# Performance work log

Measured on AMD Instinct MI355X. Metric: run time of the kernel, lower is better.

Reference implementation:

```python
import jax, jax.numpy as jnp
import numpy as np

B, LP, LH, D, H = 32, 1024, 1024, 256, 256

def setup_inputs() -> dict:
    key = jax.random.key(0)
    k1, k2, k3 = jax.random.split(key, 3)
    premises = jax.random.normal(k1, (B, LP, D), dtype=jnp.float32)
    hypotheses = jax.random.normal(k2, (B, LH, D), dtype=jnp.float32)
    W_F = jax.random.normal(k3, (D, H), dtype=jnp.float32) * (1.0 / np.sqrt(D))
    return {"premises": premises, "hypotheses": hypotheses, "W_F": W_F}

def reference(premises, hypotheses, W_F):
    # Tanh-projected features: F_p = tanh(P @ W_F), F_h = tanh(H @ W_F)
    F_p = jnp.tanh(jnp.einsum('bpd,dh->bph', premises, W_F))   # [B,LP,H]
    F_h = jnp.tanh(jnp.einsum('bqd,dh->bqh', hypotheses, W_F)) # [B,LH,H]
    # Alignment scores e_ij = F_p . F_h
    eijs = jnp.einsum('bph,bqh->bpq', F_p, F_h)                # [B,LP,LH]
    # betas: for each premise token, softmax over hypothesis tokens, weighted sum of hypotheses
    betas = jnp.einsum('bpq,bqd->bpd', jax.nn.softmax(eijs, axis=-1), hypotheses)  # [B,LP,D]
    # alphas: for each hypothesis token, softmax over premise tokens, weighted sum of premises
    alphas = jnp.einsum('bqp,bpd->bqd',
                        jax.nn.softmax(jnp.swapaxes(eijs, 1, 2), axis=-1),
                        premises)                                                   # [B,LH,D]
    return betas, alphas
```

## Files before the change

kernel.cpp:

```cpp
#include <hip/hip_runtime.h>

typedef _Float16 f16;
typedef __attribute__((ext_vector_type(4))) _Float16 f16x4;
typedef __attribute__((ext_vector_type(8))) _Float16 f16x8;
typedef __attribute__((ext_vector_type(4))) float f32x4;
typedef __attribute__((ext_vector_type(16))) float f32x16;
typedef unsigned int u32;

#define BB 32
#define LL 1024
#define DD 256

__device__ __forceinline__ void async_copy16(const f16* g, f16* l) {
  __builtin_amdgcn_global_load_lds(
      (const __attribute__((address_space(1))) u32*)(const void*)g,
      (__attribute__((address_space(3))) u32*)(void*)l, 16, 0, 0);
}

__device__ __forceinline__ u32 pack_pkrtz(float a, float b) {
  auto pk = __builtin_amdgcn_cvt_pkrtz(a, b);
  u32 w;
  __builtin_memcpy(&w, &pk, 4);
  return w;
}

__global__ __launch_bounds__(256) void transpose_to_f16(
    const float* __restrict__ X0, f16* __restrict__ Y0,
    const float* __restrict__ X1, f16* __restrict__ Y1,
    int L, int D, int nbPerInput) {
  __shared__ float T[64][68];
  const int tid = threadIdx.x;
  int bz = blockIdx.z;
  const float* X = X0;
  f16* Y = Y0;
  int b = bz;
  if (bz >= nbPerInput) { X = X1; Y = Y1; b = bz - nbPerInput; }
  const int l0 = blockIdx.x * 64, d0 = blockIdx.y * 64;
  const size_t baseX = (size_t)b * L * D;
#pragma unroll
  for (int pass = 0; pass < 4; ++pass) {
    int r = (tid >> 4) + pass * 16;
    int c = (tid & 15) * 4;
    float4 v = *(const float4*)&X[baseX + (size_t)(l0 + r) * D + d0 + c];
    *(float4*)&T[r][c] = v;
  }
  __syncthreads();
  const size_t baseY = (size_t)b * D * L;
#pragma unroll
  for (int pass = 0; pass < 2; ++pass) {
    int dr = (tid >> 3) + pass * 32;
    int lc = (tid & 7) * 8;
    f16x8 o;
#pragma unroll
    for (int j = 0; j < 8; ++j) o[j] = (f16)T[lc + j][dr];
    *(f16x8*)&Y[baseY + (size_t)(d0 + dr) * L + l0 + lc] = o;
  }
}

__global__ __launch_bounds__(256, 2) void proj_mfma(
    const float* __restrict__ Pin, const float* __restrict__ Hin,
    const f16* __restrict__ Wt, f16* __restrict__ Fp, f16* __restrict__ Fh,
    f16* __restrict__ Vtp, f16* __restrict__ Vth) {
  __shared__ f16 As[64][264];
  __shared__ f16 Wts[64][264];
  const int tid = threadIdx.x;
  const int wv = tid >> 6, lane = tid & 63, quad = lane >> 4, l16 = lane & 15;
  const float* A = blockIdx.z ? Hin : Pin;
  f16* F = blockIdx.z ? Fh : Fp;
  f16* VtO = blockIdx.z ? Vth : Vtp;
  const int m0 = blockIdx.x * 64;

  {
    const int ar = tid >> 2, aq = tid & 3;
    const float* arow = A + (size_t)(m0 + ar) * 256 + aq * 64;
    f16* drow = &As[ar][aq * 64];
#pragma unroll
    for (int i = 0; i < 16; ++i) {
      float4 v = *(const float4*)&arow[i * 4];
      f16x4 bv;
      bv[0] = (f16)v.x; bv[1] = (f16)v.y; bv[2] = (f16)v.z; bv[3] = (f16)v.w;
      *(f16x4*)&drow[i * 4] = bv;
    }
  }
  __syncthreads();

  f16x8 af[8];
#pragma unroll
  for (int kc = 0; kc < 4; ++kc)
#pragma unroll
    for (int s = 0; s < 2; ++s)
      af[kc * 2 + s] =
          *(const f16x8*)&As[wv * 16 + l16][kc * 64 + s * 32 + quad * 8];

  {
    const int dd = tid & 63, lg = tid >> 6;
    const int bI = m0 >> 10, l_base = m0 & 1023;
#pragma unroll
    for (int kc = 0; kc < 4; ++kc) {
      f16* vrow =
          VtO + (size_t)bI * DD * LL + (size_t)(kc * 64 + dd) * LL + l_base;
#pragma unroll
      for (int part = 0; part < 2; ++part) {
        int lo = lg * 16 + part * 8;
        f16x8 ov;
#pragma unroll
        for (int j = 0; j < 8; ++j) ov[j] = As[lo + j][kc * 64 + dd];
        *(f16x8*)&vrow[lo] = ov;
      }
    }
  }

  for (int nc = 0; nc < 4; ++nc) {
    __syncthreads();
#pragma unroll
    for (int pass = 0; pass < 8; ++pass) {
      int row = (tid >> 5) + pass * 8;
      int chunk = tid & 31;
      *(f16x8*)&Wts[row][chunk * 8] =
          *(const f16x8*)&Wt[(size_t)(nc * 64 + row) * 256 + chunk * 8];
    }
    __syncthreads();
    f32x4 acc[4] = {};
#pragma unroll
    for (int kc = 0; kc < 4; ++kc)
#pragma unroll
      for (int s = 0; s < 2; ++s) {
#pragma unroll
        for (int t = 0; t < 4; ++t) {
          f16x8 wf =
              *(const f16x8*)&Wts[t * 16 + l16][kc * 64 + s * 32 + quad * 8];
          acc[t] = __builtin_amdgcn_mfma_f32_16x16x32_f16(af[kc * 2 + s], wf,
                                                          acc[t], 0, 0, 0);
        }
      }
#pragma unroll
    for (int t = 0; t < 4; ++t)
#pragma unroll
      for (int r = 0; r < 4; ++r) {
        float x = acc[t][r];
        float e = __expf(2.f * x);
        float th = 1.f - 2.f / (e + 1.f);
        F[(size_t)(m0 + wv * 16 + quad * 4 + r) * 256 + nc * 64 + t * 16 +
          l16] = (f16)th;
      }
  }
}

__global__ __launch_bounds__(256, 2) void flash_mfma(
    const f16* __restrict__ Fpm, const f16* __restrict__ Fhm,
    const f16* __restrict__ Vth, const f16* __restrict__ Vtp,
    float* __restrict__ Out) {
  __shared__ f16 Kf[2][16][512];
  __shared__ f16 Vf[2][16][512];

  const int tid = threadIdx.x;
  const int wv = tid >> 6, lane = tid & 63;
  const int l32 = lane & 31, half = lane >> 5;

  const f16* Fq = Fpm;
  const f16* Fk = Fhm;
  const f16* Vt = Vth;
  float* O = Out;
  if (blockIdx.y) { Fq = Fhm; Fk = Fpm; Vt = Vtp; O = Out + (size_t)BB * LL * DD; }

  const int x = blockIdx.x;
  const int b = ((x & 7) << 2) | (x >> 6);
  const int p0 = ((x >> 3) & 7) * 128 + wv * 32;
  const int p = p0 + l32;

  const f16* Fq_b = Fq + (size_t)b * LL * DD;
  const f16* Fk_b = Fk + (size_t)b * LL * DD;
  const f16* Vt_b = Vt + (size_t)b * DD * LL;

  f16x8 qf[16];
  {
    const f16* qrow = Fq_b + (size_t)p * DD + half * 8;
#pragma unroll
    for (int s = 0; s < 16; ++s) qf[s] = *(const f16x8*)&qrow[s * 16];
  }

  float m_run = -1e30f, l_run = 0.f;
  f32x16 o[8];
#pragma unroll
  for (int t = 0; t < 8; ++t) o[t] = (f32x16)(0.f);

  auto stage = [&](int buf, int q0) {
#pragma unroll
    for (int i = 0; i < 4; ++i) {
      int s = wv * 4 + i;
      async_copy16(Fk_b + (size_t)(q0 + l32) * DD + s * 16 + half * 8,
                   &Kf[buf][s][0]);
    }
#pragma unroll
    for (int i = 0; i < 4; ++i) {
      int v = wv * 4 + i;
      int t = v >> 1, h = v & 1;
      async_copy16(Vt_b + (size_t)(t * 32 + l32) * LL + q0 + h * 16 + half * 8,
                   &Vf[buf][v][0]);
    }
  };

  stage(0, 0);
  __syncthreads();

  int cur = 0;
  for (int it = 0; it < LL / 32; ++it) {
    if (it + 1 < LL / 32) stage(cur ^ 1, (it + 1) * 32);

    f32x16 S = (f32x16)(0.f);
#pragma unroll
    for (int s = 0; s < 16; ++s) {
      f16x8 kf = *(const f16x8*)&Kf[cur][s][lane * 8];
      S = __builtin_amdgcn_mfma_f32_32x32x16_f16(kf, qf[s], S, 0, 0, 0);
    }

    float mt = S[0];
#pragma unroll
    for (int r = 1; r < 16; ++r) mt = fmaxf(mt, S[r]);
    mt = fmaxf(mt, __shfl_xor(mt, 32, 64));

    const bool keep = __all((int)(mt - m_run <= 8.0f)) != 0;
    const float mn = keep ? m_run : fmaxf(m_run, mt);
    float pe[16];
    float ts = 0.f;
#pragma unroll
    for (int r = 0; r < 16; ++r) {
      pe[r] = __expf(S[r] - mn);
      ts += pe[r];
    }
    ts += __shfl_xor(ts, 32, 64);
    if (!keep) {
      const float alpha = __expf(m_run - mn);
      l_run *= alpha;
      m_run = mn;
#pragma unroll
      for (int t = 0; t < 8; ++t)
#pragma unroll
        for (int r = 0; r < 16; ++r) o[t][r] *= alpha;
    }
    l_run += ts;

    u32 pw[8];
#pragma unroll
    for (int i = 0; i < 8; ++i) pw[i] = pack_pkrtz(pe[2 * i], pe[2 * i + 1]);
    u32 rc[4];
    {
      u32 s0 = half ? pw[0] : pw[2];
      u32 s1 = half ? pw[1] : pw[3];
      u32 s2 = half ? pw[4] : pw[6];
      u32 s3 = half ? pw[5] : pw[7];
      rc[0] = (u32)__shfl_xor((int)s0, 32, 64);
      rc[1] = (u32)__shfl_xor((int)s1, 32, 64);
      rc[2] = (u32)__shfl_xor((int)s2, 32, 64);
      rc[3] = (u32)__shfl_xor((int)s3, 32, 64);
    }
    f16x8 pf[2];
#pragma unroll
    for (int h = 0; h < 2; ++h) {
      u32 tmp[4];
      tmp[0] = half ? rc[2 * h] : pw[4 * h];
      tmp[1] = half ? rc[2 * h + 1] : pw[4 * h + 1];
      tmp[2] = half ? pw[4 * h + 2] : rc[2 * h];
      tmp[3] = half ? pw[4 * h + 3] : rc[2 * h + 1];
      __builtin_memcpy(&pf[h], tmp, 16);
    }

#pragma unroll
    for (int t = 0; t < 8; ++t) {
      f16x8 v0 = *(const f16x8*)&Vf[cur][t * 2][lane * 8];
      o[t] = __builtin_amdgcn_mfma_f32_32x32x16_f16(v0, pf[0], o[t], 0, 0, 0);
      f16x8 v1 = *(const f16x8*)&Vf[cur][t * 2 + 1][lane * 8];
      o[t] = __builtin_amdgcn_mfma_f32_32x32x16_f16(v1, pf[1], o[t], 0, 0, 0);
    }

    __syncthreads();
    cur ^= 1;
  }

  const float inv = 1.f / l_run;
  float* orow = O + ((size_t)b * LL + p) * DD;
#pragma unroll
  for (int t = 0; t < 8; ++t) {
#pragma unroll
    for (int g = 0; g < 4; ++g) {
      f32x4 v;
      v[0] = o[t][4 * g + 0] * inv;
      v[1] = o[t][4 * g + 1] * inv;
      v[2] = o[t][4 * g + 2] * inv;
      v[3] = o[t][4 * g + 3] * inv;
      *(f32x4*)&orow[t * 32 + 8 * g + 4 * half] = v;
    }
  }
}

extern "C" void kernel_launch(void* const* d_in, const int* in_sizes, int n_in,
                              void* d_out, int out_size, void* d_ws,
                              size_t ws_size, hipStream_t stream) {
  const float* premises = (const float*)d_in[0];
  const float* hypotheses = (const float*)d_in[1];
  const float* W = (const float*)d_in[2];
  float* out = (float*)d_out;

  const size_t MF = (size_t)BB * LL * DD;
  f16* Fp = (f16*)d_ws;
  f16* Fh = Fp + MF;
  f16* Vth = Fh + MF;
  f16* Vtp = Vth + MF;
  f16* Wt = (f16*)((char*)d_out + (size_t)out_size * 4 - 256 * 256 * 2);

  transpose_to_f16<<<dim3(4, 4, 1), 256, 0, stream>>>(W, Wt, W, Wt, 256, 256, 1);
  proj_mfma<<<dim3(512, 1, 2), 256, 0, stream>>>(premises, hypotheses, Wt, Fp,
                                                 Fh, Vtp, Vth);
  flash_mfma<<<dim3(256, 2), 256, 0, stream>>>(Fp, Fh, Vth, Vtp, out);
}
```

Baseline: 251.1 us.

## Use 32x32 MFMA in projection, explicit vmcnt pipelining and staged output stores in flash

The projection kernel switches from 16x16x32 to 32x32x16 MFMA with a 2x2 wave tiling, changes the LDS padding and reorganizes the input load. The flash kernel replaces the per-iteration __syncthreads with explicit vmcnt waits plus raw s_barrier so the async prefetch of the next tile overlaps compute, and adds s_setprio around MFMA sections. The output epilogue goes through LDS so global stores are row-coalesced. These target LDS traffic, barrier stalls and scattered stores, at the risk of subtle sync ordering bugs (the vmcnt count must match the number of outstanding loads) and LDS bank conflicts from the 258 padding.

Measured after the change: 227.1 us. 1.11x faster.

```diff
diff --git a/kernel.cpp b/kernel.cpp
--- a/kernel.cpp
+++ b/kernel.cpp
@@ -10,6 +10,9 @@
 #define BB 32
 #define LL 1024
 #define DD 256
+
+#define VMCNT(N) asm volatile("s_waitcnt vmcnt(" #N ")" ::: "memory")
+#define LGKMCNT0 asm volatile("s_waitcnt lgkmcnt(0)" ::: "memory")
 
 __device__ __forceinline__ void async_copy16(const f16* g, f16* l) {
   __builtin_amdgcn_global_load_lds(
@@ -61,36 +64,37 @@
     const float* __restrict__ Pin, const float* __restrict__ Hin,
     const f16* __restrict__ Wt, f16* __restrict__ Fp, f16* __restrict__ Fh,
     f16* __restrict__ Vtp, f16* __restrict__ Vth) {
-  __shared__ f16 As[64][264];
-  __shared__ f16 Wts[64][264];
+  __shared__ f16 As[64][258];
+  __shared__ f16 Wts[64][258];
   const int tid = threadIdx.x;
-  const int wv = tid >> 6, lane = tid & 63, quad = lane >> 4, l16 = lane & 15;
+  const int wv = tid >> 6, lane = tid & 63;
+  const int l32 = lane & 31, half = lane >> 5;
+  const int wm = wv >> 1, wn = wv & 1;
   const float* A = blockIdx.z ? Hin : Pin;
   f16* F = blockIdx.z ? Fh : Fp;
   f16* VtO = blockIdx.z ? Vth : Vtp;
   const int m0 = blockIdx.x * 64;
 
   {
-    const int ar = tid >> 2, aq = tid & 3;
-    const float* arow = A + (size_t)(m0 + ar) * 256 + aq * 64;
-    f16* drow = &As[ar][aq * 64];
-#pragma unroll
-    for (int i = 0; i < 16; ++i) {
-      float4 v = *(const float4*)&arow[i * 4];
-      f16x4 bv;
-      bv[0] = (f16)v.x; bv[1] = (f16)v.y; bv[2] = (f16)v.z; bv[3] = (f16)v.w;
-      *(f16x4*)&drow[i * 4] = bv;
-    }
+    const int r = tid >> 4;
+    const int c4 = (tid & 15) * 4;
+#pragma unroll
+    for (int p = 0; p < 4; ++p)
+#pragma unroll
+      for (int ch = 0; ch < 4; ++ch) {
+        float4 v =
+            *(const float4*)&A[(size_t)(m0 + r + p * 16) * 256 + ch * 64 + c4];
+        f16x4 h4;
+        h4[0] = (f16)v.x; h4[1] = (f16)v.y; h4[2] = (f16)v.z; h4[3] = (f16)v.w;
+        *(f16x4*)&As[r + p * 16][ch * 64 + c4] = h4;
+      }
   }
   __syncthreads();
 
-  f16x8 af[8];
-#pragma unroll
-  for (int kc = 0; kc < 4; ++kc)
-#pragma unroll
-    for (int s = 0; s < 2; ++s)
-      af[kc * 2 + s] =
-          *(const f16x8*)&As[wv * 16 + l16][kc * 64 + s * 32 + quad * 8];
+  f16x8 af[16];
+#pragma unroll
+  for (int ks = 0; ks < 16; ++ks)
+    af[ks] = *(const f16x8*)&As[wm * 32 + l32][ks * 16 + half * 8];
 
   {
     const int dd = tid & 63, lg = tid >> 6;
@@ -120,29 +124,20 @@
           *(const f16x8*)&Wt[(size_t)(nc * 64 + row) * 256 + chunk * 8];
     }
     __syncthreads();
-    f32x4 acc[4] = {};
-#pragma unroll
-    for (int kc = 0; kc < 4; ++kc)
-#pragma unroll
-      for (int s = 0; s < 2; ++s) {
-#pragma unroll
-        for (int t = 0; t < 4; ++t) {
-          f16x8 wf =
-              *(const f16x8*)&Wts[t * 16 + l16][kc * 64 + s * 32 + quad * 8];
-          acc[t] = __builtin_amdgcn_mfma_f32_16x16x32_f16(af[kc * 2 + s], wf,
-                                                          acc[t], 0, 0, 0);
-        }
-      }
-#pragma unroll
-    for (int t = 0; t < 4; ++t)
-#pragma unroll
-      for (int r = 0; r < 4; ++r) {
-        float x = acc[t][r];
-        float e = __expf(2.f * x);
-        float th = 1.f - 2.f / (e + 1.f);
-        F[(size_t)(m0 + wv * 16 + quad * 4 + r) * 256 + nc * 64 + t * 16 +
-          l16] = (f16)th;
-      }
+    f32x16 acc = (f32x16)(0.f);
+#pragma unroll
+    for (int ks = 0; ks < 16; ++ks) {
+      f16x8 wf = *(const f16x8*)&Wts[wn * 32 + l32][ks * 16 + half * 8];
+      acc = __builtin_amdgcn_mfma_f32_32x32x16_f16(af[ks], wf, acc, 0, 0, 0);
+    }
+#pragma unroll
+    for (int r = 0; r < 16; ++r) {
+      float x = acc[r];
+      float e = __expf(2.f * x);
+      float th = 1.f - 2.f / (e + 1.f);
+      F[(size_t)(m0 + wm * 32 + (r & 3) + 8 * (r >> 2) + 4 * half) * 256 +
+        nc * 64 + wn * 32 + l32] = (f16)th;
+    }
   }
 }
 
@@ -200,19 +195,15 @@
     }
   };
 
-  stage(0, 0);
-  __syncthreads();
-
-  int cur = 0;
-  for (int it = 0; it < LL / 32; ++it) {
-    if (it + 1 < LL / 32) stage(cur ^ 1, (it + 1) * 32);
-
+  auto tile_compute = [&](int cur) {
     f32x16 S = (f32x16)(0.f);
+    __builtin_amdgcn_s_setprio(1);
 #pragma unroll
     for (int s = 0; s < 16; ++s) {
       f16x8 kf = *(const f16x8*)&Kf[cur][s][lane * 8];
       S = __builtin_amdgcn_mfma_f32_32x32x16_f16(kf, qf[s], S, 0, 0, 0);
     }
+    __builtin_amdgcn_s_setprio(0);
 
     float mt = S[0];
 #pragma unroll
@@ -265,6 +256,7 @@
       __builtin_memcpy(&pf[h], tmp, 16);
     }
 
+    __builtin_amdgcn_s_setprio(1);
 #pragma unroll
     for (int t = 0; t < 8; ++t) {
       f16x8 v0 = *(const f16x8*)&Vf[cur][t * 2][lane * 8];
@@ -272,24 +264,50 @@
       f16x8 v1 = *(const f16x8*)&Vf[cur][t * 2 + 1][lane * 8];
       o[t] = __builtin_amdgcn_mfma_f32_32x32x16_f16(v1, pf[1], o[t], 0, 0, 0);
     }
-
-    __syncthreads();
+    __builtin_amdgcn_s_setprio(0);
+  };
+
+  stage(0, 0);
+  int cur = 0;
+  for (int it = 0; it < 31; ++it) {
+    stage(cur ^ 1, (it + 1) * 32);
+    VMCNT(8);
+    __builtin_amdgcn_sched_barrier(0);
+    __builtin_amdgcn_s_barrier();
+    tile_compute(cur);
+    __builtin_amdgcn_s_barrier();
     cur ^= 1;
   }
+  VMCNT(0);
+  __builtin_amdgcn_sched_barrier(0);
+  __builtin_amdgcn_s_barrier();
+  tile_compute(cur);
+  __syncthreads();
 
   const float inv = 1.f / l_run;
-  float* orow = O + ((size_t)b * LL + p) * DD;
+  float* Tw = (float*)&Kf[0][0][0] + wv * (32 * 36);
+  float* Ob = O + (size_t)b * LL * DD;
 #pragma unroll
   for (int t = 0; t < 8; ++t) {
 #pragma unroll
     for (int g = 0; g < 4; ++g) {
+      int C = 2 * g + half;
       f32x4 v;
       v[0] = o[t][4 * g + 0] * inv;
       v[1] = o[t][4 * g + 1] * inv;
       v[2] = o[t][4 * g + 2] * inv;
       v[3] = o[t][4 * g + 3] * inv;
-      *(f32x4*)&orow[t * 32 + 8 * g + 4 * half] = v;
-    }
+      *(f32x4*)&Tw[l32 * 36 + C * 4] = v;
+    }
+    LGKMCNT0;
+#pragma unroll
+    for (int pass = 0; pass < 4; ++pass) {
+      int row = pass * 8 + (lane >> 3);
+      int Cr = lane & 7;
+      f32x4 v = *(const f32x4*)&Tw[row * 36 + Cr * 4];
+      *(f32x4*)&Ob[(size_t)(p0 + row) * DD + t * 32 + Cr * 4] = v;
+    }
+    LGKMCNT0;
   }
 }
 
```
